# Optimization experiments

Hardware: AMD Instinct MI355X
Metric: run time of the kernel (lower is better)

Reference implementation:

```python
import jax, jax.numpy as jnp
import numpy as np

N, E, F, ED, H, C, B = 50000, 200000, 768, 768, 256, 3, 4096


def setup_inputs() -> dict:
    key = jax.random.key(0)
    ks = jax.random.split(key, 20)
    s = 0.05  # init scale for params
    inp = {
        "x": jax.random.normal(ks[0], (N, F), jnp.float32),
        "edge_attr": jax.random.normal(ks[1], (E, ED), jnp.float32),
        # GATConv layer 1 (in=F, out=H, heads=1, edge_dim=ED)
        "W1": jax.random.normal(ks[2], (F, H), jnp.float32) * s,
        "as1": jax.random.normal(ks[3], (H,), jnp.float32) * s,
        "ad1": jax.random.normal(ks[4], (H,), jnp.float32) * s,
        "We1": jax.random.normal(ks[5], (ED, H), jnp.float32) * s,
        "ae1": jax.random.normal(ks[6], (H,), jnp.float32) * s,
        "b1": jnp.zeros((H,), jnp.float32),
        # GATConv layer 2 (in=H, out=H)
        "W2": jax.random.normal(ks[7], (H, H), jnp.float32) * s,
        "as2": jax.random.normal(ks[8], (H,), jnp.float32) * s,
        "ad2": jax.random.normal(ks[9], (H,), jnp.float32) * s,
        "We2": jax.random.normal(ks[10], (ED, H), jnp.float32) * s,
        "ae2": jax.random.normal(ks[11], (H,), jnp.float32) * s,
        "b2": jnp.zeros((H,), jnp.float32),
        # prediction head
        "Wp": jax.random.normal(ks[12], (H, C), jnp.float32) * s,
        "bp": jnp.zeros((C,), jnp.float32),
        "edge_index": jax.random.randint(ks[13], (2, E), 0, N, jnp.int32),
        "nodes": jax.random.randint(ks[14], (2, B), 0, N, jnp.int32),
    }
    return inp


def gat_conv(x, edge_attr, src, dst, W, a_src, a_dst, We, a_e, b, n):
    # GATConv, heads=1, edge_dim attention, add_self_loops=False
    xl = x @ W  # [n, H]
    alpha_src = (xl * a_src).sum(-1)  # [n]
    alpha_dst = (xl * a_dst).sum(-1)  # [n]
    alpha_edge = ((edge_attr @ We) * a_e).sum(-1)  # [E]
    alpha = alpha_src[src] + alpha_dst[dst] + alpha_edge  # [E]
    alpha = jax.nn.leaky_relu(alpha, 0.2)
    # scatter-softmax over incoming edges of each destination node
    m = jax.ops.segment_max(alpha, dst, num_segments=n)
    e = jnp.exp(alpha - m[dst])
    den = jax.ops.segment_sum(e, dst, num_segments=n)
    coef = e / den[dst]  # [E]
    out = jax.ops.segment_sum(coef[:, None] * xl[src], dst, num_segments=n)
    return out + b


def reference(x, edge_attr, W1, as1, ad1, We1, ae1, b1, W2, as2, ad2, We2, ae2, b2, Wp, bp, edge_index, nodes):
    src, dst = edge_index[0], edge_index[1]
    n = x.shape[0]
    h = jax.nn.relu(gat_conv(x, edge_attr, src, dst, W1, as1, ad1, We1, ae1, b1, n))
    titles = gat_conv(h, edge_attr, src, dst, W2, as2, ad2, We2, ae2, b2, n)
    c = titles[nodes[0]] * titles[nodes[1]]  # [B, H]
    return c @ Wp + bp
```

## Files before the change

kernel.cpp:

```cpp
#include <hip/hip_runtime.h>
#include <math.h>

#define HDIM 256
#define FDIM 768
#define BM 128
#define BK 32

typedef __attribute__((ext_vector_type(8))) short short8;
typedef __attribute__((ext_vector_type(4))) float f32x4;
typedef __attribute__((ext_vector_type(4))) unsigned short us4;

__device__ __forceinline__ unsigned short f2bf(float f) {
  unsigned int u = __float_as_uint(f);
  unsigned int r = (u + 0x7FFFu + ((u >> 16) & 1u)) >> 16;
  return (unsigned short)r;
}
__device__ __forceinline__ float bf2f(unsigned short b) {
  return __uint_as_float(((unsigned int)b) << 16);
}

__device__ __forceinline__ void gload_lds16(const void* g, void* l) {
  __builtin_amdgcn_global_load_lds(
      (const __attribute__((address_space(1))) void*)g,
      (__attribute__((address_space(3))) void*)l, 16, 0, 0);
}


__device__ __forceinline__ void transpose_tile(const float* __restrict__ W,
                                               unsigned short* __restrict__ Wt,
                                               int K, int tk, int tn,
                                               float (*sT)[65], int t) {
  int lane = t & 63, rg = t >> 6;
  #pragma unroll
  for (int i = 0; i < 16; ++i) {
    int r = rg * 16 + i;
    sT[lane][r] = W[(size_t)(tk * 64 + r) * HDIM + tn * 64 + lane];
  }
  __syncthreads();
  #pragma unroll
  for (int i = 0; i < 16; ++i) {
    int h = rg * 16 + i;
    Wt[(size_t)(tn * 64 + h) * K + tk * 64 + lane] = f2bf(sT[h][lane]);
  }
}

__global__ __launch_bounds__(256) void k_prep(
    const float* __restrict__ We1, const float* __restrict__ ae1,
    const float* __restrict__ We2, const float* __restrict__ ae2,
    float* __restrict__ v1, float* __restrict__ v2,
    const float* __restrict__ W1, unsigned short* __restrict__ W1t,
    const float* __restrict__ W2, unsigned short* __restrict__ W2t,
    const int* __restrict__ dstArr, int* __restrict__ cnt, int E) {
  __shared__ float sT[64][65];
  int bid = blockIdx.x;
  int t = threadIdx.x;
  if (bid < 384) {
    int row = bid * 4 + (t >> 6);
    int lane = t & 63;
    const float* W = (row < FDIM) ? We1 : We2;
    const float* a = (row < FDIM) ? ae1 : ae2;
    int r = (row < FDIM) ? row : row - FDIM;
    float4 w = *(const float4*)&W[(size_t)r * HDIM + lane * 4];
    float4 av = *(const float4*)&a[lane * 4];
    float p = w.x * av.x + w.y * av.y + w.z * av.z + w.w * av.w;
    #pragma unroll
    for (int off = 32; off; off >>= 1) p += __shfl_down(p, off, 64);
    if (lane == 0) ((row < FDIM) ? v1 : v2)[r] = p;
  } else if (bid < 432) {
    int tile = bid - 384;
    transpose_tile(W1, W1t, FDIM, tile % 12, tile / 12, sT, t);
  } else if (bid < 448) {
    int tile = bid - 432;
    transpose_tile(W2, W2t, HDIM, tile & 3, tile >> 2, sT, t);
  } else {
    int e = (bid - 448) * 256 + t;
    if (e < E) atomicAdd(&cnt[dstArr[e]], 1);
  }
}


__global__ __launch_bounds__(256) void k_scan_lb(const int* __restrict__ cnt,
                                                 int* __restrict__ offsets,
                                                 int* __restrict__ cursor,
                                                 int* __restrict__ bsums,
                                                 int* __restrict__ flags, int n) {
  __shared__ int s[256];
  __shared__ int r[256];
  const int b = blockIdx.x, t = threadIdx.x;
  int i = b * 256 + t;
  int v = (i < n) ? cnt[i] : 0;
  s[t] = v;
  __syncthreads();
  for (int off = 1; off < 256; off <<= 1) {
    int tv = (t >= off) ? s[t - off] : 0;
    __syncthreads();
    s[t] += tv;
    __syncthreads();
  }
  if (t == 255) {
    bsums[b] = s[255];
    __threadfence();
    __hip_atomic_store(&flags[b], 1, __ATOMIC_RELEASE, __HIP_MEMORY_SCOPE_AGENT);
  }
  int contrib = 0;
  if (t < b) {
    while (!__hip_atomic_load(&flags[t], __ATOMIC_ACQUIRE, __HIP_MEMORY_SCOPE_AGENT))
      __builtin_amdgcn_s_sleep(2);
    contrib = bsums[t];
  }
  r[t] = contrib;
  __syncthreads();
  #pragma unroll
  for (int off = 128; off; off >>= 1) {
    if (t < off) r[t] += r[t + off];
    __syncthreads();
  }
  int base = r[0];
  if (i < n) {
    int incl = base + s[t];
    offsets[i + 1] = incl;
    cursor[i] = incl - v;
    if (i == 0) offsets[0] = 0;
  }
}


template <bool AF32, bool COUTBF>
__device__ __forceinline__ void gemm_body(unsigned char* lds,
                                          const void* __restrict__ Ain,
                                          const unsigned short* __restrict__ Bt,
                                          void* __restrict__ Cout,
                                          float* __restrict__ sOut,
                                          float* __restrict__ dOut,
                                          const float* __restrict__ a_src,
                                          const float* __restrict__ a_dst,
                                          int M, int K, int tile) {
  unsigned char* As = lds;
  unsigned char* Bs = lds + 8192;
  float* partS = (float*)(lds + 24576);
  float* partD = (float*)(lds + 24576 + 2048);
  const int t = threadIdx.x;
  const int l = t & 63;
  const int w = t >> 6;
  const int wm = w >> 2, wn = w & 3;
  const int bm = tile * BM;

  f32x4 acc[4][4] = {};

  int rowA = bm + (t & 127);
  if (rowA >= M) rowA = M - 1;
  const int cA = t >> 7;
  int rowAr = bm + (t >> 2);
  if (rowAr >= M) rowAr = M - 1;
  const int kbAr = t & 3;
  const int sAr = kbAr * 2048 + (t >> 2) * 16;
  const int nB = t & 255;
  const int cB0 = t >> 8;
  const int cB1 = 2 + (t >> 8);

  int aAddr[4], bAddr[4];
  #pragma unroll
  for (int mt = 0; mt < 4; ++mt) {
    int m = wm * 64 + mt * 16 + (l & 15);
    aAddr[mt] = (l >> 4) * 2048 + m * 16;
  }
  #pragma unroll
  for (int nt = 0; nt < 4; ++nt) {
    int nn = wn * 64 + nt * 16 + (l & 15);
    bAddr[nt] = (l >> 4) * 4096 + nn * 16;
  }

  const int nsteps = K / BK;
  for (int ks = 0; ks < nsteps; ++ks) {
    const int k0 = ks * BK;
    __syncthreads();
    if (AF32) {
      const float* A = (const float*)Ain;
      const float* p = A + (size_t)rowAr * K + k0 + kbAr * 8;
      float4 f0 = *(const float4*)p;
      float4 f1 = *(const float4*)(p + 4);
      short8 hv;
      hv[0] = (short)f2bf(f0.x); hv[1] = (short)f2bf(f0.y);
      hv[2] = (short)f2bf(f0.z); hv[3] = (short)f2bf(f0.w);
      hv[4] = (short)f2bf(f1.x); hv[5] = (short)f2bf(f1.y);
      hv[6] = (short)f2bf(f1.z); hv[7] = (short)f2bf(f1.w);
      *(short8*)(As + sAr) = hv;
    } else {
      const unsigned short* A = (const unsigned short*)Ain;
      gload_lds16(A + (size_t)rowA * K + k0 + cA * 8, As + t * 16);
    }
    gload_lds16(Bt + (size_t)nB * K + k0 + cB0 * 8, Bs + t * 16);
    gload_lds16(Bt + (size_t)nB * K + k0 + cB1 * 8, Bs + 8192 + t * 16);
    __syncthreads();

    short8 af[4], bfr[4];
    #pragma unroll
    for (int mt = 0; mt < 4; ++mt) af[mt] = *(const short8*)(As + aAddr[mt]);
    #pragma unroll
    for (int nt = 0; nt < 4; ++nt) bfr[nt] = *(const short8*)(Bs + bAddr[nt]);
    #pragma unroll
    for (int mt = 0; mt < 4; ++mt)
      #pragma unroll
      for (int nt = 0; nt < 4; ++nt)
        acc[mt][nt] = __builtin_amdgcn_mfma_f32_16x16x32_bf16(af[mt], bfr[nt], acc[mt][nt], 0, 0, 0);
  }

  float asv[4], adv[4];
  #pragma unroll
  for (int nt = 0; nt < 4; ++nt) {
    int col = wn * 64 + nt * 16 + (l & 15);
    asv[nt] = a_src[col];
    adv[nt] = a_dst[col];
  }
  #pragma unroll
  for (int mt = 0; mt < 4; ++mt) {
    int rloc = wm * 64 + mt * 16 + ((l >> 4) << 2);
    #pragma unroll
    for (int r = 0; r < 4; ++r) {
      int row = bm + rloc + r;
      float ps = 0.f, pd = 0.f;
      #pragma unroll
      for (int nt = 0; nt < 4; ++nt) {
        float v = acc[mt][nt][r];
        if (row < M) {
          int col = wn * 64 + nt * 16 + (l & 15);
          if (COUTBF)
            ((unsigned short*)Cout)[(size_t)row * HDIM + col] = f2bf(v);
          else
            ((float*)Cout)[(size_t)row * HDIM + col] = v;
        }
        ps += v * asv[nt];
        pd += v * adv[nt];
      }
      #pragma unroll
      for (int off = 1; off < 16; off <<= 1) {
        ps += __shfl_xor(ps, off, 64);
        pd += __shfl_xor(pd, off, 64);
      }
      if ((l & 15) == 0) {
        partS[wn * 128 + rloc + r] = ps;
        partD[wn * 128 + rloc + r] = pd;
      }
    }
  }
  __syncthreads();
  if (t < 128) {
    int row = bm + t;
    if (row < M) {
      sOut[row] = partS[t] + partS[128 + t] + partS[256 + t] + partS[384 + t];
      dOut[row] = partD[t] + partD[128 + t] + partD[256 + t] + partD[384 + t];
    }
  }
}


__device__ __forceinline__ void edge_body(unsigned char* lds,
                                          const float* __restrict__ ea,
                                          const float* __restrict__ v1,
                                          const float* __restrict__ v2,
                                          float* __restrict__ o1,
                                          float* __restrict__ o2, int E, int ebid) {
  float* sv1 = (float*)lds;
  float* sv2 = (float*)(lds + 3072);
  for (int i = threadIdx.x; i < FDIM; i += 512) { sv1[i] = v1[i]; sv2[i] = v2[i]; }
  __syncthreads();
  int lane = threadIdx.x & 63;
  int base = ebid * 32 + (threadIdx.x >> 6) * 4;
  #pragma unroll
  for (int q = 0; q < 4; ++q) {
    int e = base + q;
    if (e >= E) break;
    const float* row = ea + (size_t)e * FDIM;
    float p1 = 0.f, p2 = 0.f;
    #pragma unroll
    for (int t = 0; t < 3; ++t) {
      int idx = t * 256 + lane * 4;
      float4 x = *(const float4*)&row[idx];
      float4 a = *(const float4*)&sv1[idx];
      float4 b = *(const float4*)&sv2[idx];
      p1 += x.x * a.x + x.y * a.y + x.z * a.z + x.w * a.w;
      p2 += x.x * b.x + x.y * b.y + x.z * b.z + x.w * b.w;
    }
    #pragma unroll
    for (int off = 32; off; off >>= 1) {
      p1 += __shfl_down(p1, off, 64);
      p2 += __shfl_down(p2, off, 64);
    }
    if (lane == 0) { o1[e] = p1; o2[e] = p2; }
  }
}


#define NSCAT 98

__global__ __launch_bounds__(512) void k_fat1(
    const float* __restrict__ x, const unsigned short* __restrict__ W1t,
    unsigned short* __restrict__ xl1b, float* __restrict__ sArr, float* __restrict__ dArr,
    const float* __restrict__ as1, const float* __restrict__ ad1, int M,
    const float* __restrict__ ea, const float* __restrict__ v1,
    const float* __restrict__ v2, float* __restrict__ ae1Arr,
    float* __restrict__ ae2Arr, int E, int nGemm,
    const int* __restrict__ dstArr, int* __restrict__ cursor,
    int* __restrict__ elist) {
  __shared__ unsigned char lds[28672];
  int bid = blockIdx.x;
  if (bid < nGemm) {
    gemm_body<true, true>(lds, x, W1t, xl1b, sArr, dArr, as1, ad1, M, FDIM, bid);
  } else if (bid < nGemm + NSCAT) {
    int sb = bid - nGemm;
    for (int e = sb * 512 + threadIdx.x; e < E; e += NSCAT * 512) {
      int p = atomicAdd(&cursor[dstArr[e]], 1);
      elist[p] = e;
    }
  } else {
    edge_body(lds, ea, v1, v2, ae1Arr, ae2Arr, E, bid - nGemm - NSCAT);
  }
}

__global__ __launch_bounds__(512) void k_gemm2(
    const unsigned short* __restrict__ hb, const unsigned short* __restrict__ W2t,
    unsigned short* __restrict__ xl2b, float* __restrict__ sArr, float* __restrict__ dArr,
    const float* __restrict__ as2, const float* __restrict__ ad2, int M) {
  __shared__ unsigned char lds[28672];
  gemm_body<false, true>(lds, hb, W2t, xl2b, sArr, dArr, as2, ad2, M, HDIM, blockIdx.x);
}


__device__ __forceinline__ void agg_node(const unsigned short* __restrict__ xlb,
                                         const float* __restrict__ sArr,
                                         float dnode,
                                         const float* __restrict__ aeArr,
                                         const int* __restrict__ src,
                                         const int* __restrict__ elist,
                                         int beg, int end, int lane,
                                         float& a0, float& a1, float& a2, float& a3) {
  float run_m = -1e30f, run_den = 0.f;
  a0 = a1 = a2 = a3 = 0.f;
  for (int c0 = beg; c0 < end; c0 += 64) {
    int j = c0 + lane;
    float al = -1e30f;
    int sj = 0;
    if (j < end) {
      int e = elist[j];
      sj = src[e];
      float a = sArr[sj] + dnode + aeArr[e];
      al = (a > 0.f) ? a : 0.2f * a;
    }
    float cm = al;
    #pragma unroll
    for (int off = 32; off; off >>= 1) cm = fmaxf(cm, __shfl_xor(cm, off, 64));
    float new_m = fmaxf(run_m, cm);
    float ev = (j < end) ? expf(al - new_m) : 0.f;
    float csum = ev;
    #pragma unroll
    for (int off = 32; off; off >>= 1) csum += __shfl_xor(csum, off, 64);
    float scale = expf(run_m - new_m);
    run_den = run_den * scale + csum;
    a0 *= scale; a1 *= scale; a2 *= scale; a3 *= scale;
    int cdeg = end - c0;
    if (cdeg > 64) cdeg = 64;
    for (int q = 0; q < cdeg; ++q) {
      float wgt = __shfl(ev, q, 64);
      int sq = __shfl(sj, q, 64);
      us4 v = *(const us4*)(xlb + (size_t)sq * HDIM + lane * 4);
      a0 += wgt * bf2f(v[0]); a1 += wgt * bf2f(v[1]);
      a2 += wgt * bf2f(v[2]); a3 += wgt * bf2f(v[3]);
    }
    run_m = new_m;
  }
  float inv = (end > beg) ? 1.f / run_den : 0.f;
  a0 *= inv; a1 *= inv; a2 *= inv; a3 *= inv;
}


__global__ __launch_bounds__(256) void k_aggregate1(const unsigned short* __restrict__ xlb,
                                                    const float* __restrict__ sArr,
                                                    const float* __restrict__ dArr,
                                                    const float* __restrict__ aeArr,
                                                    const int* __restrict__ src,
                                                    const int* __restrict__ offsets,
                                                    const int* __restrict__ elist,
                                                    const float* __restrict__ bias,
                                                    unsigned short* __restrict__ outb,
                                                    int n) {
  int node = blockIdx.x * 4 + (threadIdx.x >> 6);
  if (node >= n) return;
  int lane = threadIdx.x & 63;
  int beg = offsets[node], end = offsets[node + 1];
  float a0, a1, a2, a3;
  agg_node(xlb, sArr, dArr[node], aeArr, src, elist, beg, end, lane, a0, a1, a2, a3);
  float4 bv = *(const float4*)(bias + lane * 4);
  float o0 = fmaxf(a0 + bv.x, 0.f), o1 = fmaxf(a1 + bv.y, 0.f);
  float o2 = fmaxf(a2 + bv.z, 0.f), o3 = fmaxf(a3 + bv.w, 0.f);
  us4 ov;
  ov[0] = f2bf(o0); ov[1] = f2bf(o1); ov[2] = f2bf(o2); ov[3] = f2bf(o3);
  *(us4*)(outb + (size_t)node * HDIM + lane * 4) = ov;
}


__global__ __launch_bounds__(256) void k_agg2head(const unsigned short* __restrict__ xl2b,
                                                  const float* __restrict__ sArr,
                                                  const float* __restrict__ dArr,
                                                  const float* __restrict__ aeArr,
                                                  const int* __restrict__ src,
                                                  const int* __restrict__ offsets,
                                                  const int* __restrict__ elist,
                                                  const float* __restrict__ b2,
                                                  const int* __restrict__ nodes,
                                                  const float* __restrict__ Wp,
                                                  const float* __restrict__ bp,
                                                  float* __restrict__ out, int Bn) {
  __shared__ float tls[2][2][HDIM];
  int wv = threadIdx.x >> 6;
  int lane = threadIdx.x & 63;
  int pl = wv >> 1;
  int side = wv & 1;
  int b = blockIdx.x * 2 + pl;
  if (b < Bn) {
    int node = nodes[side * Bn + b];
    int beg = offsets[node], end = offsets[node + 1];
    float a0, a1, a2, a3;
    agg_node(xl2b, sArr, dArr[node], aeArr, src, elist, beg, end, lane, a0, a1, a2, a3);
    float4 bv = *(const float4*)(b2 + lane * 4);
    float* dstp = &tls[pl][side][lane * 4];
    dstp[0] = a0 + bv.x; dstp[1] = a1 + bv.y;
    dstp[2] = a2 + bv.z; dstp[3] = a3 + bv.w;
  }
  __syncthreads();
  if (b < Bn && side == 0) {
    float4 t0 = *(const float4*)&tls[pl][0][lane * 4];
    float4 t1 = *(const float4*)&tls[pl][1][lane * 4];
    float c0 = t0.x * t1.x, c1 = t0.y * t1.y, c2 = t0.z * t1.z, c3 = t0.w * t1.w;
    int h0 = lane * 4;
    float s0 = c0 * Wp[h0 * 3 + 0] + c1 * Wp[(h0 + 1) * 3 + 0] +
               c2 * Wp[(h0 + 2) * 3 + 0] + c3 * Wp[(h0 + 3) * 3 + 0];
    float s1 = c0 * Wp[h0 * 3 + 1] + c1 * Wp[(h0 + 1) * 3 + 1] +
               c2 * Wp[(h0 + 2) * 3 + 1] + c3 * Wp[(h0 + 3) * 3 + 1];
    float s2 = c0 * Wp[h0 * 3 + 2] + c1 * Wp[(h0 + 1) * 3 + 2] +
               c2 * Wp[(h0 + 2) * 3 + 2] + c3 * Wp[(h0 + 3) * 3 + 2];
    #pragma unroll
    for (int off = 32; off; off >>= 1) {
      s0 += __shfl_down(s0, off, 64);
      s1 += __shfl_down(s1, off, 64);
      s2 += __shfl_down(s2, off, 64);
    }
    if (lane == 0) {
      out[b * 3 + 0] = s0 + bp[0];
      out[b * 3 + 1] = s1 + bp[1];
      out[b * 3 + 2] = s2 + bp[2];
    }
  }
}


extern "C" void kernel_launch(void* const* d_in, const int* in_sizes, int n_in,
                              void* d_out, int out_size, void* d_ws, size_t ws_size,
                              hipStream_t stream) {
  const float* x         = (const float*)d_in[0];
  const float* edge_attr = (const float*)d_in[1];
  const float* W1  = (const float*)d_in[2];
  const float* as1 = (const float*)d_in[3];
  const float* ad1 = (const float*)d_in[4];
  const float* We1 = (const float*)d_in[5];
  const float* ae1 = (const float*)d_in[6];
  const float* b1  = (const float*)d_in[7];
  const float* W2  = (const float*)d_in[8];
  const float* as2 = (const float*)d_in[9];
  const float* ad2 = (const float*)d_in[10];
  const float* We2 = (const float*)d_in[11];
  const float* ae2 = (const float*)d_in[12];
  const float* b2  = (const float*)d_in[13];
  const float* Wp  = (const float*)d_in[14];
  const float* bp  = (const float*)d_in[15];
  const int* edge_index = (const int*)d_in[16];
  const int* nodes      = (const int*)d_in[17];

  const int N  = in_sizes[0] / FDIM;
  const int E  = in_sizes[16] / 2;
  const int Bn = in_sizes[17] / 2;
  const int* srcArr = edge_index;
  const int* dstArr = edge_index + E;

  char* w = (char*)d_ws;
  auto carve = [&](size_t bytes) -> void* {
    void* p = (void*)w;
    w += (bytes + 255) & ~(size_t)255;
    return p;
  };
  unsigned short* xl1b   = (unsigned short*)carve(2 * (size_t)N * HDIM);
  unsigned short* hb     = (unsigned short*)carve(2 * (size_t)N * HDIM);
  unsigned short* W1t    = (unsigned short*)carve(2 * (size_t)FDIM * HDIM);
  unsigned short* W2t    = (unsigned short*)carve(2 * (size_t)HDIM * HDIM);
  float* ae1Arr = (float*)carve(sizeof(float) * E);
  float* ae2Arr = (float*)carve(sizeof(float) * E);
  float* sArr = (float*)carve(sizeof(float) * N);
  float* dArr = (float*)carve(sizeof(float) * N);
  float* v1 = (float*)carve(sizeof(float) * FDIM);
  float* v2 = (float*)carve(sizeof(float) * FDIM);
  int* cntflags = (int*)carve(sizeof(int) * (N + 256));
  int* offsets = (int*)carve(sizeof(int) * (N + 1));
  int* cursor  = (int*)carve(sizeof(int) * N);
  int* elist   = (int*)carve(sizeof(int) * E);
  int* bsums   = (int*)carve(sizeof(int) * 256);

  int* cnt = cntflags;
  int* flags = cntflags + N;

  const int nbScan = (N + 255) / 256;
  const int nbHist = (E + 255) / 256;
  const int nGemm = (N + BM - 1) / BM;
  const int nEdge = (E + 31) / 32;

  hipMemsetAsync(cntflags, 0, sizeof(int) * (N + 256), stream);
  k_prep<<<448 + nbHist, 256, 0, stream>>>(We1, ae1, We2, ae2, v1, v2,
                                           W1, W1t, W2, W2t, dstArr, cnt, E);
  k_scan_lb<<<nbScan, 256, 0, stream>>>(cnt, offsets, cursor, bsums, flags, N);

  k_fat1<<<nGemm + NSCAT + nEdge, 512, 0, stream>>>(
      x, W1t, xl1b, sArr, dArr, as1, ad1, N,
      edge_attr, v1, v2, ae1Arr, ae2Arr, E, nGemm, dstArr, cursor, elist);
  k_aggregate1<<<(N + 3) / 4, 256, 0, stream>>>(xl1b, sArr, dArr, ae1Arr, srcArr,
                                                offsets, elist, b1, hb, N);
  k_gemm2<<<nGemm, 512, 0, stream>>>(hb, W2t, xl1b, sArr, dArr, as2, ad2, N);
  k_agg2head<<<(Bn + 1) / 2, 256, 0, stream>>>(xl1b, sArr, dArr, ae2Arr, srcArr,
                                               offsets, elist, b2, nodes, Wp, bp,
                                               (float*)d_out, Bn);
}
```

Before: 276.0 us.

## Aggregate each node with a 16-lane group instead of a full wavefront

The per-node softmax aggregation now uses 16-lane subgroups, each lane holding 16 accumulators (four 64-element strides), so one wave processes four nodes at once instead of one. With an average in-degree of about four, most of a 64-lane wave's edge lanes sat idle before, and shuffle reductions shrink to four steps. The cost is more registers per lane and a serial gather loop per group that can diverge on high-degree nodes. The prediction-head kernel is remapped the same way, eight pairs per block.

```diff
diff --git a/kernel.cpp b/kernel.cpp
--- a/kernel.cpp
+++ b/kernel.cpp
@@ -326,50 +326,58 @@
 }
 
 
-__device__ __forceinline__ void agg_node(const unsigned short* __restrict__ xlb,
-                                         const float* __restrict__ sArr,
-                                         float dnode,
-                                         const float* __restrict__ aeArr,
-                                         const int* __restrict__ src,
-                                         const int* __restrict__ elist,
-                                         int beg, int end, int lane,
-                                         float& a0, float& a1, float& a2, float& a3) {
+__device__ __forceinline__ void agg_node16(const unsigned short* __restrict__ xlb,
+                                           const float* __restrict__ sArr,
+                                           float dnode,
+                                           const float* __restrict__ aeArr,
+                                           const int* __restrict__ src,
+                                           const int* __restrict__ elist,
+                                           int beg, int end, int gl, float* a) {
   float run_m = -1e30f, run_den = 0.f;
-  a0 = a1 = a2 = a3 = 0.f;
-  for (int c0 = beg; c0 < end; c0 += 64) {
-    int j = c0 + lane;
+  #pragma unroll
+  for (int i = 0; i < 16; ++i) a[i] = 0.f;
+  for (int c0 = beg; c0 < end; c0 += 16) {
+    int j = c0 + gl;
     float al = -1e30f;
     int sj = 0;
     if (j < end) {
       int e = elist[j];
       sj = src[e];
-      float a = sArr[sj] + dnode + aeArr[e];
-      al = (a > 0.f) ? a : 0.2f * a;
+      float aa = sArr[sj] + dnode + aeArr[e];
+      al = (aa > 0.f) ? aa : 0.2f * aa;
     }
     float cm = al;
     #pragma unroll
-    for (int off = 32; off; off >>= 1) cm = fmaxf(cm, __shfl_xor(cm, off, 64));
+    for (int off = 8; off; off >>= 1) cm = fmaxf(cm, __shfl_xor(cm, off, 16));
     float new_m = fmaxf(run_m, cm);
     float ev = (j < end) ? expf(al - new_m) : 0.f;
-    float csum = ev;
-    #pragma unroll
-    for (int off = 32; off; off >>= 1) csum += __shfl_xor(csum, off, 64);
+    float cs = ev;
+    #pragma unroll
+    for (int off = 8; off; off >>= 1) cs += __shfl_xor(cs, off, 16);
     float scale = expf(run_m - new_m);
-    run_den = run_den * scale + csum;
-    a0 *= scale; a1 *= scale; a2 *= scale; a3 *= scale;
+    run_den = run_den * scale + cs;
+    #pragma unroll
+    for (int i = 0; i < 16; ++i) a[i] *= scale;
     int cdeg = end - c0;
-    if (cdeg > 64) cdeg = 64;
+    if (cdeg > 16) cdeg = 16;
     for (int q = 0; q < cdeg; ++q) {
-      float wgt = __shfl(ev, q, 64);
-      int sq = __shfl(sj, q, 64);
-      us4 v = *(const us4*)(xlb + (size_t)sq * HDIM + lane * 4);
-      a0 += wgt * bf2f(v[0]); a1 += wgt * bf2f(v[1]);
-      a2 += wgt * bf2f(v[2]); a3 += wgt * bf2f(v[3]);
+      float wgt = __shfl(ev, q, 16);
+      int sq = __shfl(sj, q, 16);
+      const unsigned short* rp = xlb + (size_t)sq * HDIM + gl * 4;
+      #pragma unroll
+      for (int s = 0; s < 4; ++s) {
+        us4 v = *(const us4*)(rp + s * 64);
+        a[s * 4 + 0] += wgt * bf2f(v[0]);
+        a[s * 4 + 1] += wgt * bf2f(v[1]);
+        a[s * 4 + 2] += wgt * bf2f(v[2]);
+        a[s * 4 + 3] += wgt * bf2f(v[3]);
+      }
     }
     run_m = new_m;
   }
   float inv = (end > beg) ? 1.f / run_den : 0.f;
-  a0 *= inv; a1 *= inv; a2 *= inv; a3 *= inv;
+  #pragma unroll
+  for (int i = 0; i < 16; ++i) a[i] *= inv;
 }
 
 
@@ -383,18 +391,24 @@
                                                     const float* __restrict__ bias,
                                                     unsigned short* __restrict__ outb,
                                                     int n) {
-  int node = blockIdx.x * 4 + (threadIdx.x >> 6);
+  int grp = threadIdx.x >> 4;
+  int gl = threadIdx.x & 15;
+  int node = blockIdx.x * 16 + grp;
   if (node >= n) return;
-  int lane = threadIdx.x & 63;
   int beg = offsets[node], end = offsets[node + 1];
-  float a0, a1, a2, a3;
-  agg_node(xlb, sArr, dArr[node], aeArr, src, elist, beg, end, lane, a0, a1, a2, a3);
-  float4 bv = *(const float4*)(bias + lane * 4);
-  float o0 = fmaxf(a0 + bv.x, 0.f), o1 = fmaxf(a1 + bv.y, 0.f);
-  float o2 = fmaxf(a2 + bv.z, 0.f), o3 = fmaxf(a3 + bv.w, 0.f);
-  us4 ov;
-  ov[0] = f2bf(o0); ov[1] = f2bf(o1); ov[2] = f2bf(o2); ov[3] = f2bf(o3);
-  *(us4*)(outb + (size_t)node * HDIM + lane * 4) = ov;
+  float a[16];
+  agg_node16(xlb, sArr, dArr[node], aeArr, src, elist, beg, end, gl, a);
+  unsigned short* orow = outb + (size_t)node * HDIM + gl * 4;
+  #pragma unroll
+  for (int s = 0; s < 4; ++s) {
+    float4 bv = *(const float4*)(bias + s * 64 + gl * 4);
+    us4 ov;
+    ov[0] = f2bf(fmaxf(a[s * 4 + 0] + bv.x, 0.f));
+    ov[1] = f2bf(fmaxf(a[s * 4 + 1] + bv.y, 0.f));
+    ov[2] = f2bf(fmaxf(a[s * 4 + 2] + bv.z, 0.f));
+    ov[3] = f2bf(fmaxf(a[s * 4 + 3] + bv.w, 0.f));
+    *(us4*)(orow + s * 64) = ov;
+  }
 }
 
 
@@ -410,41 +424,51 @@
                                                   const float* __restrict__ Wp,
                                                   const float* __restrict__ bp,
                                                   float* __restrict__ out, int Bn) {
-  __shared__ float tls[2][2][HDIM];
-  int wv = threadIdx.x >> 6;
-  int lane = threadIdx.x & 63;
-  int pl = wv >> 1;
-  int side = wv & 1;
-  int b = blockIdx.x * 2 + pl;
+  __shared__ float tls[8][2][HDIM];
+  int grp = threadIdx.x >> 4;
+  int gl = threadIdx.x & 15;
+  int pl = grp >> 1;
+  int side = grp & 1;
+  int b = blockIdx.x * 8 + pl;
   if (b < Bn) {
     int node = nodes[side * Bn + b];
     int beg = offsets[node], end = offsets[node + 1];
-    float a0, a1, a2, a3;
-    agg_node(xl2b, sArr, dArr[node], aeArr, src, elist, beg, end, lane, a0, a1, a2, a3);
-    float4 bv = *(const float4*)(b2 + lane * 4);
-    float* dstp = &tls[pl][side][lane * 4];
-    dstp[0] = a0 + bv.x; dstp[1] = a1 + bv.y;
-    dstp[2] = a2 + bv.z; dstp[3] = a3 + bv.w;
+    float a[16];
+    agg_node16(xl2b, sArr, dArr[node], aeArr, src, elist, beg, end, gl, a);
+    #pragma unroll
+    for (int s = 0; s < 4; ++s) {
+      int h = s * 64 + gl * 4;
+      float4 bv = *(const float4*)(b2 + h);
+      float* dstp = &tls[pl][side][h];
+      dstp[0] = a[s * 4 + 0] + bv.x;
+      dstp[1] = a[s * 4 + 1] + bv.y;
+      dstp[2] = a[s * 4 + 2] + bv.z;
+      dstp[3] = a[s * 4 + 3] + bv.w;
+    }
   }
   __syncthreads();
   if (b < Bn && side == 0) {
-    float4 t0 = *(const float4*)&tls[pl][0][lane * 4];
-    float4 t1 = *(const float4*)&tls[pl][1][lane * 4];
-    float c0 = t0.x * t1.x, c1 = t0.y * t1.y, c2 = t0.z * t1.z, c3 = t0.w * t1.w;
-    int h0 = lane * 4;
-    float s0 = c0 * Wp[h0 * 3 + 0] + c1 * Wp[(h0 + 1) * 3 + 0] +
-               c2 * Wp[(h0 + 2) * 3 + 0] + c3 * Wp[(h0 + 3) * 3 + 0];
-    float s1 = c0 * Wp[h0 * 3 + 1] + c1 * Wp[(h0 + 1) * 3 + 1] +
-               c2 * Wp[(h0 + 2) * 3 + 1] + c3 * Wp[(h0 + 3) * 3 + 1];
-    float s2 = c0 * Wp[h0 * 3 + 2] + c1 * Wp[(h0 + 1) * 3 + 2] +
-               c2 * Wp[(h0 + 2) * 3 + 2] + c3 * Wp[(h0 + 3) * 3 + 2];
-    #pragma unroll
-    for (int off = 32; off; off >>= 1) {
-      s0 += __shfl_down(s0, off, 64);
-      s1 += __shfl_down(s1, off, 64);
-      s2 += __shfl_down(s2, off, 64);
-    }
-    if (lane == 0) {
+    float s0 = 0.f, s1 = 0.f, s2 = 0.f;
+    #pragma unroll
+    for (int s = 0; s < 4; ++s) {
+      int h = s * 64 + gl * 4;
+      float4 t0 = *(const float4*)&tls[pl][0][h];
+      float4 t1 = *(const float4*)&tls[pl][1][h];
+      float c0 = t0.x * t1.x, c1 = t0.y * t1.y, c2 = t0.z * t1.z, c3 = t0.w * t1.w;
+      s0 += c0 * Wp[h * 3 + 0] + c1 * Wp[(h + 1) * 3 + 0] +
+            c2 * Wp[(h + 2) * 3 + 0] + c3 * Wp[(h + 3) * 3 + 0];
+      s1 += c0 * Wp[h * 3 + 1] + c1 * Wp[(h + 1) * 3 + 1] +
+            c2 * Wp[(h + 2) * 3 + 1] + c3 * Wp[(h + 3) * 3 + 1];
+      s2 += c0 * Wp[h * 3 + 2] + c1 * Wp[(h + 1) * 3 + 2] +
+            c2 * Wp[(h + 2) * 3 + 2] + c3 * Wp[(h + 3) * 3 + 2];
+    }
+    #pragma unroll
+    for (int off = 8; off; off >>= 1) {
+      s0 += __shfl_down(s0, off, 16);
+      s1 += __shfl_down(s1, off, 16);
+      s2 += __shfl_down(s2, off, 16);
+    }
+    if (gl == 0) {
       out[b * 3 + 0] = s0 + bp[0];
       out[b * 3 + 1] = s1 + bp[1];
       out[b * 3 + 2] = s2 + bp[2];
@@ -519,10 +543,10 @@
   k_fat1<<<nGemm + NSCAT + nEdge, 512, 0, stream>>>(
       x, W1t, xl1b, sArr, dArr, as1, ad1, N,
       edge_attr, v1, v2, ae1Arr, ae2Arr, E, nGemm, dstArr, cursor, elist);
-  k_aggregate1<<<(N + 3) / 4, 256, 0, stream>>>(xl1b, sArr, dArr, ae1Arr, srcArr,
-                                                offsets, elist, b1, hb, N);
+  k_aggregate1<<<(N + 15) / 16, 256, 0, stream>>>(xl1b, sArr, dArr, ae1Arr, srcArr,
+                                                  offsets, elist, b1, hb, N);
   k_gemm2<<<nGemm, 512, 0, stream>>>(hb, W2t, xl1b, sArr, dArr, as2, ad2, N);
-  k_agg2head<<<(Bn + 1) / 2, 256, 0, stream>>>(xl1b, sArr, dArr, ae2Arr, srcArr,
+  k_agg2head<<<(Bn + 7) / 8, 256, 0, stream>>>(xl1b, sArr, dArr, ae2Arr, srcArr,
                                                offsets, elist, b2, nodes, Wp, bp,
                                                (float*)d_out, Bn);
 }
```

Measured after the change: 266.0 us. 1.04x faster.
